# Performance work log

Hardware: AMD Instinct MI355X
Metric: run time of the kernel (lower is better)

The kernel has to match this reference:

```python
import jax, jax.numpy as jnp
import numpy as np

N_NODES = 100000
N_EDGES = 1600000
G_DIM, H1_DIM, H2_DIM = 128, 64, 64
N_REL = 8          # 2 * n_speakers**2, n_speakers=2
N_BASES = 30


def setup_inputs() -> dict:
    key = jax.random.key(0)
    ks = jax.random.split(key, 12)
    sc = lambda *s: 1.0 / np.sqrt(s[0])
    return {
        "node_features": jax.random.normal(ks[0], (N_NODES, G_DIM), jnp.float32),
        "edge_index": jax.random.randint(ks[1], (2, N_EDGES), 0, N_NODES),
        "edge_norm": jax.random.uniform(ks[2], (N_EDGES,), jnp.float32),
        "edge_type": jax.random.randint(ks[3], (N_EDGES,), 0, N_REL),
        # RGCNConv params (basis decomposition)
        "basis": jax.random.normal(ks[4], (N_BASES, G_DIM, H1_DIM), jnp.float32) * sc(G_DIM),
        "comp": jax.random.normal(ks[5], (N_REL, N_BASES), jnp.float32) * sc(N_BASES),
        "root": jax.random.normal(ks[6], (G_DIM, H1_DIM), jnp.float32) * sc(G_DIM),
        "bias1": jnp.zeros((H1_DIM,), jnp.float32),
        # GraphConv params
        "w_rel": jax.random.normal(ks[7], (H1_DIM, H2_DIM), jnp.float32) * sc(H1_DIM),
        "b_rel": jnp.zeros((H2_DIM,), jnp.float32),
        "w_root": jax.random.normal(ks[8], (H1_DIM, H2_DIM), jnp.float32) * sc(H1_DIM),
    }


def reference(node_features, edge_index, edge_norm, edge_type,
              basis, comp, root, bias1, w_rel, b_rel, w_root):
    N = node_features.shape[0]
    src, dst = edge_index[0], edge_index[1]

    # ---- RGCNConv: per-relation mean aggregation, basis-decomposed weights ----
    W = jnp.einsum('rb,bio->rio', comp, basis)          # [R, g, h1]
    x_src = node_features[src]                           # [E, g] gather
    out1 = node_features @ root + bias1                  # root + bias
    for r in range(N_REL):                               # fixed small relation set
        m = (edge_type == r).astype(node_features.dtype)  # [E]
        s = jax.ops.segment_sum(x_src * m[:, None], dst, num_segments=N)  # [N, g]
        cnt = jax.ops.segment_sum(m, dst, num_segments=N)                 # [N]
        h = s / jnp.maximum(cnt, 1.0)[:, None]            # mean aggr (0 if no edges)
        out1 = out1 + h @ W[r]

    # ---- GraphConv: sum of x_j * edge_weight -> lin_rel, plus lin_root ----
    agg = jax.ops.segment_sum(out1[src] * edge_norm[:, None], dst, num_segments=N)
    out2 = agg @ w_rel + b_rel + out1 @ w_root
    return out2
```

## Files before the change

kernel.cpp:

```cpp
#include <hip/hip_runtime.h>
#include <hip/hip_bf16.h>

#define NN 100000
#define NE 1600000
#define GD 128
#define H1 64
#define H2 64
#define NREL 8
#define NBASES 30
#define NBTOT 576

#define NPB 256
#define NBUCK ((NN + NPB - 1) / NPB)
#define NWGA 128
#define ECHUNK ((NE + NWGA - 1) / NWGA)

typedef __attribute__((ext_vector_type(8))) short bf16x8;
typedef __attribute__((ext_vector_type(4))) float f32x4;

static __device__ __forceinline__ unsigned short f2bf(float x) {
    __hip_bfloat16 h = __float2bfloat16(x);
    return *reinterpret_cast<unsigned short*>(&h);
}
static __device__ __forceinline__ float bf2f(unsigned short u) {
    return __uint_as_float(((unsigned)u) << 16);
}

__global__ void prep_kernel(const float* __restrict__ basis,
                            const float* __restrict__ comp,
                            const float* __restrict__ root,
                            const float* __restrict__ w_rel,
                            const float* __restrict__ w_root,
                            unsigned short* __restrict__ WcatT,
                            unsigned short* __restrict__ B2T)
{
    int idx = blockIdx.x * blockDim.x + threadIdx.x;
    const int totalW = NBTOT * GD;
    if (idx < totalW) {
        int c = idx / GD;
        int i = idx % GD;
        float v;
        if (c < NREL * H1) {
            int r = c >> 6, o = c & 63;
            float acc = 0.f;
            #pragma unroll 5
            for (int b = 0; b < NBASES; ++b)
                acc += comp[r * NBASES + b] * basis[(b * GD + i) * H1 + o];
            v = acc;
        } else {
            v = root[i * H1 + (c - NREL * H1)];
        }
        WcatT[idx] = f2bf(v);
    } else {
        int j = idx - totalW;
        if (j < H2 * GD) {
            int o = j / GD, i = j % GD;
            float v = (i < H1) ? w_rel[i * H2 + o] : w_root[(i - H1) * H2 + o];
            B2T[j] = f2bf(v);
        }
    }
}

__global__ __launch_bounds__(512)
void bucket_count(const int* __restrict__ ei, unsigned* __restrict__ bcnt)
{
    __shared__ unsigned l[NBUCK];
    int t = threadIdx.x;
    int c0 = blockIdx.x * ECHUNK;
    int c1 = c0 + ECHUNK; if (c1 > NE) c1 = NE;
    for (int i = t; i < NBUCK; i += 512) l[i] = 0;
    __syncthreads();
    for (int e = c0 + t; e < c1; e += 512)
        atomicAdd(&l[ei[NE + e] >> 8], 1u);
    __syncthreads();
    for (int i = t; i < NBUCK; i += 512)
        if (l[i]) atomicAdd(&bcnt[i], l[i]);
}

__global__ __launch_bounds__(512)
void bucket_scan(const unsigned* __restrict__ bcnt,
                 unsigned* __restrict__ boff,
                 unsigned* __restrict__ bcur,
                 unsigned* __restrict__ off)
{
    __shared__ unsigned s[512];
    int t = threadIdx.x;
    unsigned v = (t < NBUCK) ? bcnt[t] : 0u;
    s[t] = v;
    __syncthreads();
    for (int st = 1; st < 512; st <<= 1) {
        unsigned u = (t >= st) ? s[t - st] : 0u;
        __syncthreads();
        s[t] += u;
        __syncthreads();
    }
    if (t < NBUCK) { boff[t] = s[t] - v; bcur[t] = s[t] - v; }
    if (t == 511) { boff[NBUCK] = s[511]; off[NN] = s[511]; }
}

__global__ __launch_bounds__(512)
void partition_a(const int* __restrict__ ei, const int* __restrict__ et,
                 const float* __restrict__ enorm,
                 unsigned* __restrict__ bcur,
                 uint2* __restrict__ tmp)
{
    __shared__ unsigned lcnt[NBUCK], wbase[NBUCK], lcur[NBUCK];
    int t = threadIdx.x;
    int c0 = blockIdx.x * ECHUNK;
    int c1 = c0 + ECHUNK; if (c1 > NE) c1 = NE;
    for (int i = t; i < NBUCK; i += 512) { lcnt[i] = 0; lcur[i] = 0; }
    __syncthreads();
    for (int e = c0 + t; e < c1; e += 512) {
        int dst = ei[NE + e];
        atomicAdd(&lcnt[dst >> 8], 1u);
    }
    __syncthreads();
    for (int i = t; i < NBUCK; i += 512)
        wbase[i] = atomicAdd(&bcur[i], lcnt[i]);
    __syncthreads();
    for (int e = c0 + t; e < c1; e += 512) {
        int src = ei[e], dst = ei[NE + e], r = et[e];
        int b = dst >> 8;
        unsigned pos = wbase[b] + atomicAdd(&lcur[b], 1u);
        unsigned dl = (unsigned)(dst & (NPB - 1));
        tmp[pos] = make_uint2((dl << 24) | ((unsigned)src << 3) | (unsigned)r,
                              __float_as_uint(enorm[e]));
    }
}

__global__ __launch_bounds__(512)
void partition_b(const unsigned* __restrict__ boff,
                 const uint2* __restrict__ tmp,
                 uint2* __restrict__ csr,
                 unsigned* __restrict__ off,
                 unsigned* __restrict__ cnt)
{
    __shared__ unsigned lcnt[NPB * NREL];
    __shared__ unsigned sscan[256];
    __shared__ unsigned lcur[NPB];
    int b = blockIdx.x, t = threadIdx.x;
    int nlo = b * NPB;
    int nn = NN - nlo; if (nn > NPB) nn = NPB;
    for (int i = t; i < NPB * NREL; i += 512) lcnt[i] = 0;
    __syncthreads();
    unsigned bstart = boff[b], bend = boff[b + 1];
    for (unsigned j = bstart + t; j < bend; j += 512) {
        unsigned x = tmp[j].x;
        atomicAdd(&lcnt[((x >> 24) << 3) | (x & 7u)], 1u);
    }
    __syncthreads();
    unsigned tot = 0;
    if (t < 256) {
        if (t < nn) {
            #pragma unroll
            for (int r = 0; r < NREL; ++r) tot += lcnt[t * NREL + r];
        }
        sscan[t] = tot;
    }
    __syncthreads();
    for (int st = 1; st < 256; st <<= 1) {
        unsigned u = (t < 256 && t >= st) ? sscan[t - st] : 0u;
        __syncthreads();
        if (t < 256) sscan[t] += u;
        __syncthreads();
    }
    if (t < nn) {
        unsigned ex = bstart + sscan[t] - tot;
        off[nlo + t] = ex;
        lcur[t] = ex;
        *reinterpret_cast<uint4*>(&cnt[(size_t)(nlo + t) * NREL]) =
            *reinterpret_cast<uint4*>(&lcnt[t * NREL]);
        *reinterpret_cast<uint4*>(&cnt[(size_t)(nlo + t) * NREL + 4]) =
            *reinterpret_cast<uint4*>(&lcnt[t * NREL + 4]);
    }
    __syncthreads();
    for (unsigned j = bstart + t; j < bend; j += 512) {
        uint2 rec = tmp[j];
        unsigned dl = rec.x >> 24;
        unsigned p = atomicAdd(&lcur[dl], 1u);
        csr[p] = make_uint2(rec.x & 0x00FFFFFFu, rec.y);
    }
}

template<int MODE>
__global__ __launch_bounds__(256)
void mfma_gemm(const void* __restrict__ Avoid,
               const unsigned short* __restrict__ Bt,
               int M,
               const float* __restrict__ bias,
               unsigned short* __restrict__ y,
               unsigned short* __restrict__ root1b,
               float* __restrict__ out)
{
    constexpr int NT = (MODE == 0) ? 9 : 1;
    __shared__ unsigned short Alds[128 * 128];
    __shared__ unsigned short Blds[64 * 128];

    int tid = threadIdx.x;
    int m0 = blockIdx.x * 128;
    int w = tid >> 6, l = tid & 63;
    int lr = l & 15, lk = l >> 4;

    uint4 breg0, breg1, breg2, breg3;
    {
        int c0 = (0 * 256 + tid) >> 4, s0 = tid & 15;
        int c1 = (1 * 256 + tid) >> 4, s1 = tid & 15;
        int c2 = (2 * 256 + tid) >> 4, s2 = tid & 15;
        int c3 = (3 * 256 + tid) >> 4, s3 = tid & 15;
        breg0 = *reinterpret_cast<const uint4*>(&Bt[(size_t)c0 * GD + s0 * 8]);
        breg1 = *reinterpret_cast<const uint4*>(&Bt[(size_t)c1 * GD + s1 * 8]);
        breg2 = *reinterpret_cast<const uint4*>(&Bt[(size_t)c2 * GD + s2 * 8]);
        breg3 = *reinterpret_cast<const uint4*>(&Bt[(size_t)c3 * GD + s3 * 8]);
    }

    if (MODE == 0) {
        const float* A = (const float*)Avoid;
        #pragma unroll
        for (int p = 0; p < 16; ++p) {
            int f = p * 256 + tid;
            int r = f >> 5;
            int c4 = f & 31;
            float4 av = make_float4(0.f, 0.f, 0.f, 0.f);
            if (m0 + r < M)
                av = *reinterpret_cast<const float4*>(&A[(size_t)(m0 + r) * GD + c4 * 4]);
            ushort4 bv;
            bv.x = f2bf(av.x); bv.y = f2bf(av.y); bv.z = f2bf(av.z); bv.w = f2bf(av.w);
            int slot = (c4 >> 1) ^ (r & 7);
            int byte = r * 256 + (slot << 4) + ((c4 & 1) << 3);
            *reinterpret_cast<ushort4*>(reinterpret_cast<char*>(Alds) + byte) = bv;
        }
    } else {
        const unsigned short* A = (const unsigned short*)Avoid;
        #pragma unroll
        for (int p = 0; p < 8; ++p) {
            int f = p * 256 + tid;
            int r = f >> 4;
            int slot = f & 15;
            uint4 v = make_uint4(0u, 0u, 0u, 0u);
            if (m0 + r < M)
                v = *reinterpret_cast<const uint4*>(&A[(size_t)(m0 + r) * GD + slot * 8]);
            int byte = r * 256 + ((slot ^ (r & 7)) << 4);
            *reinterpret_cast<uint4*>(reinterpret_cast<char*>(Alds) + byte) = v;
        }
    }

    {
        int c = (0 * 256 + tid) >> 4, s = tid & 15;
        *reinterpret_cast<uint4*>(reinterpret_cast<char*>(Blds) + c * 256 + ((s ^ (c & 7)) << 4)) = breg0;
        c = (1 * 256 + tid) >> 4;
        *reinterpret_cast<uint4*>(reinterpret_cast<char*>(Blds) + c * 256 + ((s ^ (c & 7)) << 4)) = breg1;
        c = (2 * 256 + tid) >> 4;
        *reinterpret_cast<uint4*>(reinterpret_cast<char*>(Blds) + c * 256 + ((s ^ (c & 7)) << 4)) = breg2;
        c = (3 * 256 + tid) >> 4;
        *reinterpret_cast<uint4*>(reinterpret_cast<char*>(Blds) + c * 256 + ((s ^ (c & 7)) << 4)) = breg3;
    }
    asm volatile("s_waitcnt lgkmcnt(0)" ::: "memory");
    __builtin_amdgcn_sched_barrier(0);
    __builtin_amdgcn_s_barrier();
    __builtin_amdgcn_sched_barrier(0);

    #pragma unroll 1
    for (int nt = 0; nt < NT; ++nt) {
        if (nt + 1 < NT) {
            int c = (0 * 256 + tid) >> 4, s = tid & 15;
            breg0 = *reinterpret_cast<const uint4*>(&Bt[(size_t)((nt + 1) * 64 + c) * GD + s * 8]);
            c = (1 * 256 + tid) >> 4;
            breg1 = *reinterpret_cast<const uint4*>(&Bt[(size_t)((nt + 1) * 64 + c) * GD + s * 8]);
            c = (2 * 256 + tid) >> 4;
            breg2 = *reinterpret_cast<const uint4*>(&Bt[(size_t)((nt + 1) * 64 + c) * GD + s * 8]);
            c = (3 * 256 + tid) >> 4;
            breg3 = *reinterpret_cast<const uint4*>(&Bt[(size_t)((nt + 1) * 64 + c) * GD + s * 8]);
        }

        f32x4 acc[2][4];
        #pragma unroll
        for (int i = 0; i < 2; ++i)
            #pragma unroll
            for (int j = 0; j < 4; ++j)
                acc[i][j] = (f32x4){0.f, 0.f, 0.f, 0.f};

        #pragma unroll
        for (int ks = 0; ks < 4; ++ks) {
            int q = 4 * ks + lk;
            int sA = q ^ (lr & 7);
            bf16x8 a0 = *reinterpret_cast<const bf16x8*>(
                reinterpret_cast<char*>(Alds) + (w * 32 + 0 * 16 + lr) * 256 + (sA << 4));
            bf16x8 a1 = *reinterpret_cast<const bf16x8*>(
                reinterpret_cast<char*>(Alds) + (w * 32 + 1 * 16 + lr) * 256 + (sA << 4));
            #pragma unroll
            for (int cf = 0; cf < 4; ++cf) {
                bf16x8 b = *reinterpret_cast<const bf16x8*>(
                    reinterpret_cast<char*>(Blds) + (cf * 16 + lr) * 256 + (sA << 4));
                acc[0][cf] = __builtin_amdgcn_mfma_f32_16x16x32_bf16(b, a0, acc[0][cf], 0, 0, 0);
                acc[1][cf] = __builtin_amdgcn_mfma_f32_16x16x32_bf16(b, a1, acc[1][cf], 0, 0, 0);
            }
        }

        #pragma unroll
        for (int rf = 0; rf < 2; ++rf) {
            int row = m0 + w * 32 + rf * 16 + lr;
            if (row < M) {
                #pragma unroll
                for (int cf = 0; cf < 4; ++cf) {
                    int cb = cf * 16 + lk * 4;
                    f32x4 v = acc[rf][cf];
                    if (MODE == 0) {
                        if (nt < 8) {
                            ushort4 pv;
                            pv.x = f2bf(v[0]); pv.y = f2bf(v[1]);
                            pv.z = f2bf(v[2]); pv.w = f2bf(v[3]);
                            *reinterpret_cast<ushort4*>(&y[(size_t)row * 512 + nt * 64 + cb]) = pv;
                        } else {
                            float4 bb = *reinterpret_cast<const float4*>(&bias[cb]);
                            ushort4 pv;
                            pv.x = f2bf(v[0] + bb.x); pv.y = f2bf(v[1] + bb.y);
                            pv.z = f2bf(v[2] + bb.z); pv.w = f2bf(v[3] + bb.w);
                            *reinterpret_cast<ushort4*>(&root1b[(size_t)row * 64 + cb]) = pv;
                        }
                    } else {
                        float4 bb = *reinterpret_cast<const float4*>(&bias[cb]);
                        float4 ov;
                        ov.x = v[0] + bb.x; ov.y = v[1] + bb.y;
                        ov.z = v[2] + bb.z; ov.w = v[3] + bb.w;
                        *reinterpret_cast<float4*>(&out[(size_t)row * 64 + cb]) = ov;
                    }
                }
            }
        }

        if (nt + 1 < NT) {
            asm volatile("s_waitcnt lgkmcnt(0)" ::: "memory");
            __builtin_amdgcn_sched_barrier(0);
            __builtin_amdgcn_s_barrier();
            __builtin_amdgcn_sched_barrier(0);
            int c = (0 * 256 + tid) >> 4, s = tid & 15;
            *reinterpret_cast<uint4*>(reinterpret_cast<char*>(Blds) + c * 256 + ((s ^ (c & 7)) << 4)) = breg0;
            c = (1 * 256 + tid) >> 4;
            *reinterpret_cast<uint4*>(reinterpret_cast<char*>(Blds) + c * 256 + ((s ^ (c & 7)) << 4)) = breg1;
            c = (2 * 256 + tid) >> 4;
            *reinterpret_cast<uint4*>(reinterpret_cast<char*>(Blds) + c * 256 + ((s ^ (c & 7)) << 4)) = breg2;
            c = (3 * 256 + tid) >> 4;
            *reinterpret_cast<uint4*>(reinterpret_cast<char*>(Blds) + c * 256 + ((s ^ (c & 7)) << 4)) = breg3;
            asm volatile("s_waitcnt lgkmcnt(0)" ::: "memory");
            __builtin_amdgcn_sched_barrier(0);
            __builtin_amdgcn_s_barrier();
            __builtin_amdgcn_sched_barrier(0);
        }
    }
}

__global__ void rgcn_aggregate(const unsigned* __restrict__ off,
                               const uint2* __restrict__ csr,
                               const unsigned* __restrict__ cnt,
                               const unsigned short* __restrict__ y,
                               const unsigned short* __restrict__ root1b,
                               unsigned short* __restrict__ abuf)
{
    int gid = blockIdx.x * blockDim.x + threadIdx.x;
    int n = gid >> 6;
    int lane = gid & 63;
    if (n >= NN) return;
    unsigned myc = (lane < NREL) ? cnt[(size_t)n * NREL + lane] : 1u;
    float myinv = 1.0f / (float)(myc > 0u ? myc : 1u);
    unsigned s = off[n], e = off[n + 1];
    float a0 = 0.f, a1 = 0.f, a2 = 0.f, a3 = 0.f;
    unsigned i = s;
    for (; i + 4 <= e; i += 4) {
        uint2 q0 = csr[i], q1 = csr[i + 1], q2 = csr[i + 2], q3 = csr[i + 3];
        float v0 = bf2f(y[(size_t)q0.x * 64 + lane]);
        float v1 = bf2f(y[(size_t)q1.x * 64 + lane]);
        float v2 = bf2f(y[(size_t)q2.x * 64 + lane]);
        float v3 = bf2f(y[(size_t)q3.x * 64 + lane]);
        a0 += v0 * __shfl(myinv, (int)(q0.x & 7));
        a1 += v1 * __shfl(myinv, (int)(q1.x & 7));
        a2 += v2 * __shfl(myinv, (int)(q2.x & 7));
        a3 += v3 * __shfl(myinv, (int)(q3.x & 7));
    }
    for (; i < e; ++i) {
        uint2 q = csr[i];
        a0 += bf2f(y[(size_t)q.x * 64 + lane]) * __shfl(myinv, (int)(q.x & 7));
    }
    float out1 = bf2f(root1b[(size_t)n * 64 + lane]) + ((a0 + a1) + (a2 + a3));
    abuf[(size_t)n * 128 + 64 + lane] = f2bf(out1);
}

__global__ void graph_aggregate(const unsigned* __restrict__ off,
                                const uint2* __restrict__ csr,
                                unsigned short* __restrict__ abuf)
{
    int gid = blockIdx.x * blockDim.x + threadIdx.x;
    int n = gid >> 6;
    int lane = gid & 63;
    if (n >= NN) return;
    unsigned s = off[n], e = off[n + 1];
    float a0 = 0.f, a1 = 0.f, a2 = 0.f, a3 = 0.f;
    unsigned i = s;
    for (; i + 4 <= e; i += 4) {
        uint2 q0 = csr[i], q1 = csr[i + 1], q2 = csr[i + 2], q3 = csr[i + 3];
        float v0 = bf2f(abuf[(size_t)(q0.x >> 3) * 128 + 64 + lane]);
        float v1 = bf2f(abuf[(size_t)(q1.x >> 3) * 128 + 64 + lane]);
        float v2 = bf2f(abuf[(size_t)(q2.x >> 3) * 128 + 64 + lane]);
        float v3 = bf2f(abuf[(size_t)(q3.x >> 3) * 128 + 64 + lane]);
        a0 += v0 * __uint_as_float(q0.y);
        a1 += v1 * __uint_as_float(q1.y);
        a2 += v2 * __uint_as_float(q2.y);
        a3 += v3 * __uint_as_float(q3.y);
    }
    for (; i < e; ++i) {
        uint2 q = csr[i];
        a0 += bf2f(abuf[(size_t)(q.x >> 3) * 128 + 64 + lane]) * __uint_as_float(q.y);
    }
    abuf[(size_t)n * 128 + lane] = f2bf(((a0 + a1) + (a2 + a3)));
}

extern "C" void kernel_launch(void* const* d_in, const int* in_sizes, int n_in,
                              void* d_out, int out_size, void* d_ws, size_t ws_size,
                              hipStream_t stream)
{
    const float* node_features = (const float*)d_in[0];
    const int*   edge_index    = (const int*)d_in[1];
    const float* edge_norm     = (const float*)d_in[2];
    const int*   edge_type     = (const int*)d_in[3];
    const float* basis         = (const float*)d_in[4];
    const float* comp          = (const float*)d_in[5];
    const float* root          = (const float*)d_in[6];
    const float* bias1         = (const float*)d_in[7];
    const float* w_rel         = (const float*)d_in[8];
    const float* b_rel         = (const float*)d_in[9];
    const float* w_root        = (const float*)d_in[10];
    float* out = (float*)d_out;

    char* ws = (char*)d_ws;
    size_t o = 0;
    auto alloc = [&](size_t bytes) -> void* {
        o = (o + 511) & ~(size_t)511;
        void* p = ws + o;
        o += bytes;
        return p;
    };
    unsigned short* WcatT = (unsigned short*)alloc((size_t)NBTOT * GD * 2);
    unsigned short* B2T   = (unsigned short*)alloc((size_t)H2 * GD * 2);
    unsigned* cnt      = (unsigned*)alloc((size_t)NN * NREL * 4);
    unsigned* off_     = (unsigned*)alloc((size_t)(NN + 1) * 4);
    unsigned* bcnt     = (unsigned*)alloc((size_t)NBUCK * 4);
    unsigned* boff     = (unsigned*)alloc((size_t)(NBUCK + 1) * 4);
    unsigned* bcur     = (unsigned*)alloc((size_t)NBUCK * 4);
    uint2*    csr      = (uint2*)alloc((size_t)NE * 8);
    unsigned short* y  = (unsigned short*)alloc((size_t)NN * 512 * 2);
    unsigned short* root1b = (unsigned short*)alloc((size_t)NN * 64 * 2);
    unsigned short* abuf = (unsigned short*)alloc((size_t)NN * 128 * 2);
    uint2*    tmp      = (uint2*)abuf;

    hipMemsetAsync(bcnt, 0, (size_t)NBUCK * 4, stream);

    prep_kernel<<<(NBTOT * GD + H2 * GD + 255) / 256, 256, 0, stream>>>(
        basis, comp, root, w_rel, w_root, WcatT, B2T);

    bucket_count<<<NWGA, 512, 0, stream>>>(edge_index, bcnt);
    bucket_scan<<<1, 512, 0, stream>>>(bcnt, boff, bcur, off_);
    partition_a<<<NWGA, 512, 0, stream>>>(edge_index, edge_type, edge_norm, bcur, tmp);
    partition_b<<<NBUCK, 512, 0, stream>>>(boff, tmp, csr, off_, cnt);

    int gblk = (NN + 127) / 128;
    mfma_gemm<0><<<gblk, 256, 0, stream>>>(node_features, WcatT, NN, bias1, y, root1b, nullptr);

    rgcn_aggregate<<<(NN * 64 + 255) / 256, 256, 0, stream>>>(off_, csr, cnt, y, root1b, abuf);

    graph_aggregate<<<(NN * 64 + 255) / 256, 256, 0, stream>>>(off_, csr, abuf);

    mfma_gemm<1><<<gblk, 256, 0, stream>>>(abuf, B2T, NN, b_rel, nullptr, nullptr, out);
}
```

Before: 296.4 us.

## Split wavefront into four edge groups with 8-byte vector gathers in aggregations

Both aggregation kernels now assign 16 lanes per edge, with each lane loading 4 bf16 values (8 bytes) of the gathered row. A wavefront therefore processes 4 edges at once instead of one edge per 64 lanes, and the partial sums are combined with xor shuffles at the end. This aims to cut the number of load instructions and the serial latency chain per node, at the cost of a cross-group reduction and masked tail handling. A trivial cleanup of the B register load indices is included.

```diff
diff --git a/kernel.cpp b/kernel.cpp
--- a/kernel.cpp
+++ b/kernel.cpp
@@ -24,6 +24,12 @@
 }
 static __device__ __forceinline__ float bf2f(unsigned short u) {
     return __uint_as_float(((unsigned)u) << 16);
+}
+static __device__ __forceinline__ float bflo(unsigned u) {
+    return __uint_as_float(u << 16);
+}
+static __device__ __forceinline__ float bfhi(unsigned u) {
+    return __uint_as_float(u & 0xffff0000u);
 }
 
 __global__ void prep_kernel(const float* __restrict__ basis,
@@ -204,13 +210,13 @@
     uint4 breg0, breg1, breg2, breg3;
     {
         int c0 = (0 * 256 + tid) >> 4, s0 = tid & 15;
-        int c1 = (1 * 256 + tid) >> 4, s1 = tid & 15;
-        int c2 = (2 * 256 + tid) >> 4, s2 = tid & 15;
-        int c3 = (3 * 256 + tid) >> 4, s3 = tid & 15;
+        int c1 = (1 * 256 + tid) >> 4;
+        int c2 = (2 * 256 + tid) >> 4;
+        int c3 = (3 * 256 + tid) >> 4;
         breg0 = *reinterpret_cast<const uint4*>(&Bt[(size_t)c0 * GD + s0 * 8]);
-        breg1 = *reinterpret_cast<const uint4*>(&Bt[(size_t)c1 * GD + s1 * 8]);
-        breg2 = *reinterpret_cast<const uint4*>(&Bt[(size_t)c2 * GD + s2 * 8]);
-        breg3 = *reinterpret_cast<const uint4*>(&Bt[(size_t)c3 * GD + s3 * 8]);
+        breg1 = *reinterpret_cast<const uint4*>(&Bt[(size_t)c1 * GD + s0 * 8]);
+        breg2 = *reinterpret_cast<const uint4*>(&Bt[(size_t)c2 * GD + s0 * 8]);
+        breg3 = *reinterpret_cast<const uint4*>(&Bt[(size_t)c3 * GD + s0 * 8]);
     }
 
     if (MODE == 0) {
@@ -358,30 +364,60 @@
 {
     int gid = blockIdx.x * blockDim.x + threadIdx.x;
     int n = gid >> 6;
-    int lane = gid & 63;
+    int l = gid & 63;
     if (n >= NN) return;
-    unsigned myc = (lane < NREL) ? cnt[(size_t)n * NREL + lane] : 1u;
+    int g = l >> 4;
+    int sl = l & 15;
+    unsigned myc = (l < NREL) ? cnt[(size_t)n * NREL + l] : 1u;
     float myinv = 1.0f / (float)(myc > 0u ? myc : 1u);
     unsigned s = off[n], e = off[n + 1];
     float a0 = 0.f, a1 = 0.f, a2 = 0.f, a3 = 0.f;
+    float b0 = 0.f, b1 = 0.f, b2 = 0.f, b3 = 0.f;
     unsigned i = s;
-    for (; i + 4 <= e; i += 4) {
-        uint2 q0 = csr[i], q1 = csr[i + 1], q2 = csr[i + 2], q3 = csr[i + 3];
-        float v0 = bf2f(y[(size_t)q0.x * 64 + lane]);
-        float v1 = bf2f(y[(size_t)q1.x * 64 + lane]);
-        float v2 = bf2f(y[(size_t)q2.x * 64 + lane]);
-        float v3 = bf2f(y[(size_t)q3.x * 64 + lane]);
-        a0 += v0 * __shfl(myinv, (int)(q0.x & 7));
-        a1 += v1 * __shfl(myinv, (int)(q1.x & 7));
-        a2 += v2 * __shfl(myinv, (int)(q2.x & 7));
-        a3 += v3 * __shfl(myinv, (int)(q3.x & 7));
-    }
-    for (; i < e; ++i) {
-        uint2 q = csr[i];
-        a0 += bf2f(y[(size_t)q.x * 64 + lane]) * __shfl(myinv, (int)(q.x & 7));
-    }
-    float out1 = bf2f(root1b[(size_t)n * 64 + lane]) + ((a0 + a1) + (a2 + a3));
-    abuf[(size_t)n * 128 + 64 + lane] = f2bf(out1);
+    for (; i + 8 <= e; i += 8) {
+        uint2 rA = csr[i + g];
+        uint2 rB = csr[i + 4 + g];
+        uint2 vA = *reinterpret_cast<const uint2*>(&y[(size_t)rA.x * 64 + sl * 4]);
+        uint2 vB = *reinterpret_cast<const uint2*>(&y[(size_t)rB.x * 64 + sl * 4]);
+        float wA = __shfl(myinv, (int)(rA.x & 7));
+        float wB = __shfl(myinv, (int)(rB.x & 7));
+        a0 += wA * bflo(vA.x); a1 += wA * bfhi(vA.x);
+        a2 += wA * bflo(vA.y); a3 += wA * bfhi(vA.y);
+        b0 += wB * bflo(vB.x); b1 += wB * bfhi(vB.x);
+        b2 += wB * bflo(vB.y); b3 += wB * bfhi(vB.y);
+    }
+    if (i + 4 <= e) {
+        uint2 rA = csr[i + g];
+        uint2 vA = *reinterpret_cast<const uint2*>(&y[(size_t)rA.x * 64 + sl * 4]);
+        float wA = __shfl(myinv, (int)(rA.x & 7));
+        a0 += wA * bflo(vA.x); a1 += wA * bfhi(vA.x);
+        a2 += wA * bflo(vA.y); a3 += wA * bfhi(vA.y);
+        i += 4;
+    }
+    if (i < e) {
+        unsigned idx = i + (unsigned)g;
+        bool valid = idx < e;
+        uint2 r = csr[valid ? idx : i];
+        uint2 v = *reinterpret_cast<const uint2*>(&y[(size_t)r.x * 64 + sl * 4]);
+        float w = __shfl(myinv, (int)(r.x & 7));
+        if (!valid) w = 0.f;
+        b0 += w * bflo(v.x); b1 += w * bfhi(v.x);
+        b2 += w * bflo(v.y); b3 += w * bfhi(v.y);
+    }
+    a0 += b0; a1 += b1; a2 += b2; a3 += b3;
+    a0 += __shfl_xor(a0, 16); a0 += __shfl_xor(a0, 32);
+    a1 += __shfl_xor(a1, 16); a1 += __shfl_xor(a1, 32);
+    a2 += __shfl_xor(a2, 16); a2 += __shfl_xor(a2, 32);
+    a3 += __shfl_xor(a3, 16); a3 += __shfl_xor(a3, 32);
+    if (g == 0) {
+        uint2 rb = *reinterpret_cast<const uint2*>(&root1b[(size_t)n * 64 + sl * 4]);
+        ushort4 pv;
+        pv.x = f2bf(bflo(rb.x) + a0);
+        pv.y = f2bf(bfhi(rb.x) + a1);
+        pv.z = f2bf(bflo(rb.y) + a2);
+        pv.w = f2bf(bfhi(rb.y) + a3);
+        *reinterpret_cast<ushort4*>(&abuf[(size_t)n * 128 + 64 + sl * 4]) = pv;
+    }
 }
 
 __global__ void graph_aggregate(const unsigned* __restrict__ off,
@@ -390,27 +426,53 @@
 {
     int gid = blockIdx.x * blockDim.x + threadIdx.x;
     int n = gid >> 6;
-    int lane = gid & 63;
+    int l = gid & 63;
     if (n >= NN) return;
+    int g = l >> 4;
+    int sl = l & 15;
     unsigned s = off[n], e = off[n + 1];
     float a0 = 0.f, a1 = 0.f, a2 = 0.f, a3 = 0.f;
+    float b0 = 0.f, b1 = 0.f, b2 = 0.f, b3 = 0.f;
     unsigned i = s;
-    for (; i + 4 <= e; i += 4) {
-        uint2 q0 = csr[i], q1 = csr[i + 1], q2 = csr[i + 2], q3 = csr[i + 3];
-        float v0 = bf2f(abuf[(size_t)(q0.x >> 3) * 128 + 64 + lane]);
-        float v1 = bf2f(abuf[(size_t)(q1.x >> 3) * 128 + 64 + lane]);
-        float v2 = bf2f(abuf[(size_t)(q2.x >> 3) * 128 + 64 + lane]);
-        float v3 = bf2f(abuf[(size_t)(q3.x >> 3) * 128 + 64 + lane]);
-        a0 += v0 * __uint_as_float(q0.y);
-        a1 += v1 * __uint_as_float(q1.y);
-        a2 += v2 * __uint_as_float(q2.y);
-        a3 += v3 * __uint_as_float(q3.y);
-    }
-    for (; i < e; ++i) {
-        uint2 q = csr[i];
-        a0 += bf2f(abuf[(size_t)(q.x >> 3) * 128 + 64 + lane]) * __uint_as_float(q.y);
-    }
-    abuf[(size_t)n * 128 + lane] = f2bf(((a0 + a1) + (a2 + a3)));
+    for (; i + 8 <= e; i += 8) {
+        uint2 rA = csr[i + g];
+        uint2 rB = csr[i + 4 + g];
+        uint2 vA = *reinterpret_cast<const uint2*>(&abuf[(size_t)(rA.x >> 3) * 128 + 64 + sl * 4]);
+        uint2 vB = *reinterpret_cast<const uint2*>(&abuf[(size_t)(rB.x >> 3) * 128 + 64 + sl * 4]);
+        float wA = __uint_as_float(rA.y);
+        float wB = __uint_as_float(rB.y);
+        a0 += wA * bflo(vA.x); a1 += wA * bfhi(vA.x);
+        a2 += wA * bflo(vA.y); a3 += wA * bfhi(vA.y);
+        b0 += wB * bflo(vB.x); b1 += wB * bfhi(vB.x);
+        b2 += wB * bflo(vB.y); b3 += wB * bfhi(vB.y);
+    }
+    if (i + 4 <= e) {
+        uint2 rA = csr[i + g];
+        uint2 vA = *reinterpret_cast<const uint2*>(&abuf[(size_t)(rA.x >> 3) * 128 + 64 + sl * 4]);
+        float wA = __uint_as_float(rA.y);
+        a0 += wA * bflo(vA.x); a1 += wA * bfhi(vA.x);
+        a2 += wA * bflo(vA.y); a3 += wA * bfhi(vA.y);
+        i += 4;
+    }
+    if (i < e) {
+        unsigned idx = i + (unsigned)g;
+        bool valid = idx < e;
+        uint2 r = csr[valid ? idx : i];
+        uint2 v = *reinterpret_cast<const uint2*>(&abuf[(size_t)(r.x >> 3) * 128 + 64 + sl * 4]);
+        float w = valid ? __uint_as_float(r.y) : 0.f;
+        b0 += w * bflo(v.x); b1 += w * bfhi(v.x);
+        b2 += w * bflo(v.y); b3 += w * bfhi(v.y);
+    }
+    a0 += b0; a1 += b1; a2 += b2; a3 += b3;
+    a0 += __shfl_xor(a0, 16); a0 += __shfl_xor(a0, 32);
+    a1 += __shfl_xor(a1, 16); a1 += __shfl_xor(a1, 32);
+    a2 += __shfl_xor(a2, 16); a2 += __shfl_xor(a2, 32);
+    a3 += __shfl_xor(a3, 16); a3 += __shfl_xor(a3, 32);
+    if (g == 0) {
+        ushort4 pv;
+        pv.x = f2bf(a0); pv.y = f2bf(a1); pv.z = f2bf(a2); pv.w = f2bf(a3);
+        *reinterpret_cast<ushort4*>(&abuf[(size_t)n * 128 + sl * 4]) = pv;
+    }
 }
 
 extern "C" void kernel_launch(void* const* d_in, const int* in_sizes, int n_in,
```

Measured after the change: 248.5 us. -16.2%, faster.
